# Optimization experiments

Measured on AMD Instinct MI355X. Metric: run time of the kernel, lower is better.

The kernel has to match this reference:

```python
import jax, jax.numpy as jnp
import numpy as np

D_MODEL = 512
EPS = 1e-5


def setup_inputs() -> dict:
    key = jax.random.key(0)
    k1, k2, k3 = jax.random.split(key, 3)
    B, N, D = 8, 2048, D_MODEL
    output = jax.random.normal(k1, (B, N, D), dtype=jnp.float32)
    # multiplicative 0/1 float mask over the [B, N, N] score matrix
    slf_attn_mask = jax.random.randint(k2, (B, N, N), 0, 2).astype(jnp.float32)
    # nn.Linear(d_model, d_model): weight [out, in], xavier-uniform; bias zeros-ish
    limit = float(np.sqrt(6.0 / (D + D)))
    W = jax.random.uniform(k3, (D, D), dtype=jnp.float32, minval=-limit, maxval=limit)
    b = jnp.zeros((D,), dtype=jnp.float32)
    return {"output": output, "slf_attn_mask": slf_attn_mask, "W": W, "b": b}


def reference(output, slf_attn_mask, W, b):
    temperature = jnp.asarray(D_MODEL, output.dtype) ** 0.5
    # scores: [B, N, N] = (q / temp) @ k^T, then multiplicative mask
    attn = jnp.einsum("bnd,bmd->bnm", output / temperature, output) * slf_attn_mask
    # F.normalize(p=2, dim=-1, eps=1e-5): x / max(||x||_2, eps)
    norm = jnp.sqrt(jnp.sum(attn * attn, axis=-1, keepdims=True))
    attn = attn / jnp.maximum(norm, EPS)
    # values: elu(Linear(output)), Linear uses W @ x + b with W [out, in]
    v = jax.nn.elu(jnp.einsum("bnd,ed->bne", output, W) + b)
    return jnp.einsum("bnm,bme->bne", attn, v)
```

## Files before the change

### kernel.cpp

```cpp
#include <hip/hip_runtime.h>
#include <hip/hip_bf16.h>

#define NSEQ 2048
#define DM 512
#define BATCH 8
#define GTOT (BATCH * NSEQ)
#define INV_T 0.044194173824159216f
#define EPSN 1e-5f

typedef __bf16 bf16_t;
typedef bf16_t bf16x8 __attribute__((ext_vector_type(8)));
typedef float f32x16 __attribute__((ext_vector_type(16)));
typedef unsigned short u16;
typedef unsigned int u32;
typedef unsigned long long u64;

__device__ __forceinline__ u16 f2bf(float f) {
    u32 u = __builtin_bit_cast(u32, f);
    u32 r = (u + 0x7FFFu + ((u >> 16) & 1u)) >> 16;
    return (u16)r;
}

__device__ __forceinline__ void async16(const u16* g, u16* l) {
    __builtin_amdgcn_global_load_lds(
        (const __attribute__((address_space(1))) u32*)g,
        (__attribute__((address_space(3))) u32*)l, 16, 0, 0);
}

__device__ __forceinline__ bf16x8 fragld(const u16* t, int row, int kc) {
    return *(const bf16x8*)(t + row * 32 + ((kc ^ ((row >> 1) & 3)) << 3));
}

#define MFMA32(a, b, c) __builtin_amdgcn_mfma_f32_32x32x16_bf16(a, b, c, 0, 0, 0)
#define ROWOFF(reg, lh) (((reg) & 3) + 8 * ((reg) >> 2) + 4 * (lh))

#define STAGE(Ag, ldA, Bg, ldB, k0)                                                    \
    do {                                                                               \
        async16((Ag) + (long)rA0 * (ldA) + (k0) + kcg * 8, Ab + u0 * 512 + lane * 8);  \
        async16((Ag) + (long)(rA0 + 16) * (ldA) + (k0) + kcg * 8, Ab + (u0 + 1) * 512 + lane * 8); \
        async16((Bg) + (long)rA0 * (ldB) + (k0) + kcg * 8, Bb + u0 * 512 + lane * 8);  \
        async16((Bg) + (long)(rA0 + 16) * (ldB) + (k0) + kcg * 8, Bb + (u0 + 1) * 512 + lane * 8); \
    } while (0)

__global__ __launch_bounds__(256) void k_convert(
    const float* __restrict__ X, const float* __restrict__ W,
    const float* __restrict__ mask,
    u16* __restrict__ Kbf, u16* __restrict__ Wbf,
    float* __restrict__ ssbuf, u64* __restrict__ Mbits) {
    const long NK = (long)GTOT * DM / 4;
    const long NW = (long)DM * DM / 4;
    const long NS = GTOT / 4;
    const long NM = (long)BATCH * NSEQ * NSEQ / 4;
    long i = (long)blockIdx.x * 256 + threadIdx.x;
    if (i < NK) {
        float4 f = ((const float4*)X)[i];
        ushort4 o;
        o.x = f2bf(f.x); o.y = f2bf(f.y); o.z = f2bf(f.z); o.w = f2bf(f.w);
        ((ushort4*)Kbf)[i] = o;
    } else if (i < NK + NW) {
        long j = i - NK;
        float4 f = ((const float4*)W)[j];
        ushort4 o;
        o.x = f2bf(f.x); o.y = f2bf(f.y); o.z = f2bf(f.z); o.w = f2bf(f.w);
        ((ushort4*)Wbf)[j] = o;
    } else if (i < NK + NW + NS) {
        ((float4*)ssbuf)[i - NK - NW] = (float4){0.f, 0.f, 0.f, 0.f};
    } else if (i < NK + NW + NS + NM) {
        long j4 = i - NK - NW - NS;
        int lane = threadIdx.x & 63;
        long wb = (j4 >> 6) << 6;
        long elembase = wb * 4;
#pragma unroll
        for (int it = 0; it < 4; ++it) {
            float f = mask[elembase + it * 64 + lane];
            u64 bb = __ballot(f != 0.f);
            if (lane == 0) Mbits[((wb >> 6) << 2) + it] = bb;
        }
    }
}

__global__ __launch_bounds__(256, 4) void k_sgemm(
    const u16* __restrict__ Kbf, const u32* __restrict__ Mw,
    u16* __restrict__ Sbuf, float* __restrict__ ssbuf) {
    __shared__ __attribute__((aligned(16))) u16 Ab[4096], Bb[4096];
    const int tid = threadIdx.x, wave = tid >> 6, lane = tid & 63;
    const int l31 = lane & 31, lh = lane >> 5;
    const int wy = wave >> 1, wx = wave & 1;
    const int b = blockIdx.z;
    const int M0 = blockIdx.y * 128, N0 = blockIdx.x * 128;
    const u16* Ag = Kbf + (long)(b * NSEQ + M0) * DM;
    const u16* Bg = Kbf + (long)(b * NSEQ + N0) * DM;
    const u32* Mb = Mw + (long)b * NSEQ * 64;

    const int u0 = wave * 2;
    const int rA0 = u0 * 16 + (lane >> 2);
    const int kcg = (lane & 3) ^ ((lane >> 3) & 3);

    f32x16 acc[2][2];
#pragma unroll
    for (int i = 0; i < 2; ++i)
#pragma unroll
        for (int j = 0; j < 2; ++j)
#pragma unroll
            for (int e = 0; e < 16; ++e) acc[i][j][e] = 0.f;

    for (int kt = 0; kt < 16; ++kt) {
        const int k0 = kt * 32;
        __syncthreads();
        STAGE(Ag, DM, Bg, DM, k0);
        __syncthreads();
#pragma unroll
        for (int ks = 0; ks < 2; ++ks) {
            const int kc = ks * 2 + lh;
            bf16x8 a0 = fragld(Ab, wy * 64 + l31, kc);
            bf16x8 a1 = fragld(Ab, wy * 64 + 32 + l31, kc);
            bf16x8 b0 = fragld(Bb, wx * 64 + l31, kc);
            bf16x8 b1 = fragld(Bb, wx * 64 + 32 + l31, kc);
            acc[0][0] = MFMA32(a0, b0, acc[0][0]);
            acc[0][1] = MFMA32(a0, b1, acc[0][1]);
            acc[1][0] = MFMA32(a1, b0, acc[1][0]);
            acc[1][1] = MFMA32(a1, b1, acc[1][1]);
        }
    }
#pragma unroll
    for (int mi = 0; mi < 2; ++mi) {
#pragma unroll
        for (int reg = 0; reg < 16; ++reg) {
            int rl = M0 + wy * 64 + mi * 32 + ROWOFF(reg, lh);
            long rg = (long)b * NSEQ + rl;
            float v = 0.f;
#pragma unroll
            for (int ni = 0; ni < 2; ++ni) {
                int cg = N0 + wx * 64 + ni * 32 + l31;
                u32 w = Mb[(long)rl * 64 + (cg >> 5)];
                float s = ((w >> l31) & 1u) ? acc[mi][ni][reg] * INV_T : 0.f;
                v += s * s;
                Sbuf[rg * NSEQ + cg] = f2bf(s);
            }
            v += __shfl_xor(v, 1, 32);
            v += __shfl_xor(v, 2, 32);
            v += __shfl_xor(v, 4, 32);
            v += __shfl_xor(v, 8, 32);
            v += __shfl_xor(v, 16, 32);
            if (l31 == 0) atomicAdd(&ssbuf[rg], v);
        }
    }
}

__global__ __launch_bounds__(256, 4) void k_vgemm(
    const u16* __restrict__ Wbf, const u16* __restrict__ Kbf,
    const float* __restrict__ bias, u16* __restrict__ vT) {
    __shared__ __attribute__((aligned(16))) u16 Ab[4096], Bb[4096];
    const int tid = threadIdx.x, wave = tid >> 6, lane = tid & 63;
    const int l31 = lane & 31, lh = lane >> 5;
    const int wy = wave >> 1, wx = wave & 1;
    const int M0 = blockIdx.y * 128, N0 = blockIdx.x * 128;
    const u16* Ag = Wbf + (long)M0 * DM;
    const u16* Bg = Kbf + (long)N0 * DM;

    const int u0 = wave * 2;
    const int rA0 = u0 * 16 + (lane >> 2);
    const int kcg = (lane & 3) ^ ((lane >> 3) & 3);

    f32x16 acc[2][2];
#pragma unroll
    for (int i = 0; i < 2; ++i)
#pragma unroll
        for (int j = 0; j < 2; ++j)
#pragma unroll
            for (int e = 0; e < 16; ++e) acc[i][j][e] = 0.f;

    for (int kt = 0; kt < 16; ++kt) {
        const int k0 = kt * 32;
        __syncthreads();
        STAGE(Ag, DM, Bg, DM, k0);
        __syncthreads();
#pragma unroll
        for (int ks = 0; ks < 2; ++ks) {
            const int kc = ks * 2 + lh;
            bf16x8 a0 = fragld(Ab, wy * 64 + l31, kc);
            bf16x8 a1 = fragld(Ab, wy * 64 + 32 + l31, kc);
            bf16x8 b0 = fragld(Bb, wx * 64 + l31, kc);
            bf16x8 b1 = fragld(Bb, wx * 64 + 32 + l31, kc);
            acc[0][0] = MFMA32(a0, b0, acc[0][0]);
            acc[0][1] = MFMA32(a0, b1, acc[0][1]);
            acc[1][0] = MFMA32(a1, b0, acc[1][0]);
            acc[1][1] = MFMA32(a1, b1, acc[1][1]);
        }
    }
#pragma unroll
    for (int mi = 0; mi < 2; ++mi) {
#pragma unroll
        for (int reg = 0; reg < 16; ++reg) {
            int e = M0 + wy * 64 + mi * 32 + ROWOFF(reg, lh);
            float bv = bias[e];
#pragma unroll
            for (int ni = 0; ni < 2; ++ni) {
                int g = N0 + wx * 64 + ni * 32 + l31;
                float x = acc[mi][ni][reg] + bv;
                float v = x > 0.f ? x : (__expf(x) - 1.f);
                vT[(long)e * GTOT + g] = f2bf(v);
            }
        }
    }
}

__global__ __launch_bounds__(256, 4) void k_pv(
    const u16* __restrict__ Sbuf, const u16* __restrict__ vT,
    const float* __restrict__ ssbuf, float* __restrict__ Out) {
    __shared__ __attribute__((aligned(16))) u16 Ab[4096], Bb[4096];
    __shared__ float sc[128];
    const int tid = threadIdx.x, wave = tid >> 6, lane = tid & 63;
    const int l31 = lane & 31, lh = lane >> 5;
    const int wy = wave >> 1, wx = wave & 1;
    const int b = blockIdx.z;
    const int M0 = blockIdx.y * 128, N0 = blockIdx.x * 128;
    const u16* Ag = Sbuf + (long)(b * NSEQ + M0) * NSEQ;
    const u16* Bg = vT + (long)N0 * GTOT + b * NSEQ;

    if (tid < 128) {
        float v = ssbuf[b * NSEQ + M0 + tid];
        sc[tid] = 1.f / fmaxf(sqrtf(v), EPSN);
    }

    const int u0 = wave * 2;
    const int rA0 = u0 * 16 + (lane >> 2);
    const int kcg = (lane & 3) ^ ((lane >> 3) & 3);

    f32x16 acc[2][2];
#pragma unroll
    for (int i = 0; i < 2; ++i)
#pragma unroll
        for (int j = 0; j < 2; ++j)
#pragma unroll
            for (int e = 0; e < 16; ++e) acc[i][j][e] = 0.f;

    for (int kt = 0; kt < 64; ++kt) {
        const int k0 = kt * 32;
        __syncthreads();
        STAGE(Ag, NSEQ, Bg, GTOT, k0);
        __syncthreads();
#pragma unroll
        for (int ks = 0; ks < 2; ++ks) {
            const int kc = ks * 2 + lh;
            bf16x8 a0 = fragld(Ab, wy * 64 + l31, kc);
            bf16x8 a1 = fragld(Ab, wy * 64 + 32 + l31, kc);
            bf16x8 b0 = fragld(Bb, wx * 64 + l31, kc);
            bf16x8 b1 = fragld(Bb, wx * 64 + 32 + l31, kc);
            acc[0][0] = MFMA32(a0, b0, acc[0][0]);
            acc[0][1] = MFMA32(a0, b1, acc[0][1]);
            acc[1][0] = MFMA32(a1, b0, acc[1][0]);
            acc[1][1] = MFMA32(a1, b1, acc[1][1]);
        }
    }
#pragma unroll
    for (int mi = 0; mi < 2; ++mi) {
#pragma unroll
        for (int reg = 0; reg < 16; ++reg) {
            int rl = wy * 64 + mi * 32 + ROWOFF(reg, lh);
            float s = sc[rl];
            float* op = Out + ((long)b * NSEQ + M0 + rl) * DM;
#pragma unroll
            for (int ni = 0; ni < 2; ++ni) {
                int d = N0 + wx * 64 + ni * 32 + l31;
                op[d] = acc[mi][ni][reg] * s;
            }
        }
    }
}

extern "C" void kernel_launch(void* const* d_in, const int* in_sizes, int n_in,
                              void* d_out, int out_size, void* d_ws, size_t ws_size,
                              hipStream_t stream) {
    const float* X = (const float*)d_in[0];
    const float* mask = (const float*)d_in[1];
    const float* W = (const float*)d_in[2];
    const float* bias = (const float*)d_in[3];
    float* out = (float*)d_out;

    char* ws = (char*)d_ws;
    u16* Kbf = (u16*)ws;
    u16* Wbf = (u16*)(ws + 16777216);
    u16* vT = (u16*)(ws + 17301504);
    u16* Sbuf = (u16*)(ws + 34078720);
    float* ssbuf = (float*)(ws + 101187584);
    u64* Mbits = (u64*)(ws + 101253120);

    k_convert<<<41232, 256, 0, stream>>>(X, W, mask, Kbf, Wbf, ssbuf, Mbits);
    k_vgemm<<<dim3(128, 4), 256, 0, stream>>>(Wbf, Kbf, bias, vT);
    k_sgemm<<<dim3(16, 16, 8), 256, 0, stream>>>(Kbf, (const u32*)Mbits, Sbuf, ssbuf);
    k_pv<<<dim3(4, 16, 8), 256, 0, stream>>>(Sbuf, vT, ssbuf, out);
}
```

Baseline: 370.9 us.

## Double GEMM K-tile to 64 and split mask packing into float4 kernel

All three bf16 MFMA GEMMs now stage 64-wide K tiles instead of 32, using a new 8-way XOR swizzle. This halves the number of barrier pairs per K loop and doubles the work done between syncs, at the cost of twice the LDS per block, which may limit occupancy. The mask bit-packing moves out of the convert kernel into its own kernel. That kernel reads float4 per thread and assembles the 64-bit words through shared-memory nibbles, replacing scalar per-lane loads with a ballot.

After: 348.1 us. 1.07x faster.

```diff
diff --git a/kernel.cpp b/kernel.cpp
--- a/kernel.cpp
+++ b/kernel.cpp
@@ -13,6 +13,7 @@
 typedef float f32x16 __attribute__((ext_vector_type(16)));
 typedef unsigned short u16;
 typedef unsigned int u32;
+typedef unsigned char u8;
 typedef unsigned long long u64;
 
 __device__ __forceinline__ u16 f2bf(float f) {
@@ -27,30 +28,29 @@
         (__attribute__((address_space(3))) u32*)l, 16, 0, 0);
 }
 
-__device__ __forceinline__ bf16x8 fragld(const u16* t, int row, int kc) {
-    return *(const bf16x8*)(t + row * 32 + ((kc ^ ((row >> 1) & 3)) << 3));
+__device__ __forceinline__ bf16x8 fragld64(const u16* t, int row, int kc) {
+    return *(const bf16x8*)(t + row * 64 + ((kc ^ ((row >> 1) & 7)) << 3));
 }
 
 #define MFMA32(a, b, c) __builtin_amdgcn_mfma_f32_32x32x16_bf16(a, b, c, 0, 0, 0)
 #define ROWOFF(reg, lh) (((reg) & 3) + 8 * ((reg) >> 2) + 4 * (lh))
 
-#define STAGE(Ag, ldA, Bg, ldB, k0)                                                    \
-    do {                                                                               \
-        async16((Ag) + (long)rA0 * (ldA) + (k0) + kcg * 8, Ab + u0 * 512 + lane * 8);  \
-        async16((Ag) + (long)(rA0 + 16) * (ldA) + (k0) + kcg * 8, Ab + (u0 + 1) * 512 + lane * 8); \
-        async16((Bg) + (long)rA0 * (ldB) + (k0) + kcg * 8, Bb + u0 * 512 + lane * 8);  \
-        async16((Bg) + (long)(rA0 + 16) * (ldB) + (k0) + kcg * 8, Bb + (u0 + 1) * 512 + lane * 8); \
+#define STAGE64(Ag, ldA, Bg, ldB, k0)                                            \
+    do {                                                                         \
+        _Pragma("unroll") for (int j = 0; j < 4; ++j) {                          \
+            const int cg = (lane & 7) ^ ((j * 4 + (lane >> 4)) & 7);             \
+            const int dst = (wave * 4 + j) * 512 + lane * 8;                     \
+            async16((Ag) + (long)(rS + j * 8) * (ldA) + (k0) + cg * 8, Ab + dst);\
+            async16((Bg) + (long)(rS + j * 8) * (ldB) + (k0) + cg * 8, Bb + dst);\
+        }                                                                        \
     } while (0)
 
 __global__ __launch_bounds__(256) void k_convert(
     const float* __restrict__ X, const float* __restrict__ W,
-    const float* __restrict__ mask,
-    u16* __restrict__ Kbf, u16* __restrict__ Wbf,
-    float* __restrict__ ssbuf, u64* __restrict__ Mbits) {
+    u16* __restrict__ Kbf, u16* __restrict__ Wbf, float* __restrict__ ssbuf) {
     const long NK = (long)GTOT * DM / 4;
     const long NW = (long)DM * DM / 4;
     const long NS = GTOT / 4;
-    const long NM = (long)BATCH * NSEQ * NSEQ / 4;
     long i = (long)blockIdx.x * 256 + threadIdx.x;
     if (i < NK) {
         float4 f = ((const float4*)X)[i];
@@ -65,24 +65,31 @@
         ((ushort4*)Wbf)[j] = o;
     } else if (i < NK + NW + NS) {
         ((float4*)ssbuf)[i - NK - NW] = (float4){0.f, 0.f, 0.f, 0.f};
-    } else if (i < NK + NW + NS + NM) {
-        long j4 = i - NK - NW - NS;
-        int lane = threadIdx.x & 63;
-        long wb = (j4 >> 6) << 6;
-        long elembase = wb * 4;
-#pragma unroll
-        for (int it = 0; it < 4; ++it) {
-            float f = mask[elembase + it * 64 + lane];
-            u64 bb = __ballot(f != 0.f);
-            if (lane == 0) Mbits[((wb >> 6) << 2) + it] = bb;
-        }
+    }
+}
+
+__global__ __launch_bounds__(256) void k_maskpack(
+    const float* __restrict__ mask, u64* __restrict__ Mbits) {
+    __shared__ u8 nib[256];
+    const int tid = threadIdx.x;
+    const long fbase = (long)blockIdx.x * 256 + tid;
+    float4 f = ((const float4*)mask)[fbase];
+    unsigned n = (f.x != 0.f ? 1u : 0u) | (f.y != 0.f ? 2u : 0u) |
+                 (f.z != 0.f ? 4u : 0u) | (f.w != 0.f ? 8u : 0u);
+    nib[tid] = (u8)n;
+    __syncthreads();
+    if (tid < 16) {
+        u64 w = 0;
+#pragma unroll
+        for (int i = 0; i < 16; ++i) w |= (u64)nib[tid * 16 + i] << (i * 4);
+        Mbits[(long)blockIdx.x * 16 + tid] = w;
     }
 }
 
 __global__ __launch_bounds__(256, 4) void k_sgemm(
     const u16* __restrict__ Kbf, const u32* __restrict__ Mw,
     u16* __restrict__ Sbuf, float* __restrict__ ssbuf) {
-    __shared__ __attribute__((aligned(16))) u16 Ab[4096], Bb[4096];
+    __shared__ __attribute__((aligned(16))) u16 Ab[8192], Bb[8192];
     const int tid = threadIdx.x, wave = tid >> 6, lane = tid & 63;
     const int l31 = lane & 31, lh = lane >> 5;
     const int wy = wave >> 1, wx = wave & 1;
@@ -92,9 +99,7 @@
     const u16* Bg = Kbf + (long)(b * NSEQ + N0) * DM;
     const u32* Mb = Mw + (long)b * NSEQ * 64;
 
-    const int u0 = wave * 2;
-    const int rA0 = u0 * 16 + (lane >> 2);
-    const int kcg = (lane & 3) ^ ((lane >> 3) & 3);
+    const int rS = wave * 32 + (lane >> 3);
 
     f32x16 acc[2][2];
 #pragma unroll
@@ -104,18 +109,18 @@
 #pragma unroll
             for (int e = 0; e < 16; ++e) acc[i][j][e] = 0.f;
 
-    for (int kt = 0; kt < 16; ++kt) {
-        const int k0 = kt * 32;
-        __syncthreads();
-        STAGE(Ag, DM, Bg, DM, k0);
-        __syncthreads();
-#pragma unroll
-        for (int ks = 0; ks < 2; ++ks) {
+    for (int kt = 0; kt < 8; ++kt) {
+        const int k0 = kt * 64;
+        __syncthreads();
+        STAGE64(Ag, DM, Bg, DM, k0);
+        __syncthreads();
+#pragma unroll
+        for (int ks = 0; ks < 4; ++ks) {
             const int kc = ks * 2 + lh;
-            bf16x8 a0 = fragld(Ab, wy * 64 + l31, kc);
-            bf16x8 a1 = fragld(Ab, wy * 64 + 32 + l31, kc);
-            bf16x8 b0 = fragld(Bb, wx * 64 + l31, kc);
-            bf16x8 b1 = fragld(Bb, wx * 64 + 32 + l31, kc);
+            bf16x8 a0 = fragld64(Ab, wy * 64 + l31, kc);
+            bf16x8 a1 = fragld64(Ab, wy * 64 + 32 + l31, kc);
+            bf16x8 b0 = fragld64(Bb, wx * 64 + l31, kc);
+            bf16x8 b1 = fragld64(Bb, wx * 64 + 32 + l31, kc);
             acc[0][0] = MFMA32(a0, b0, acc[0][0]);
             acc[0][1] = MFMA32(a0, b1, acc[0][1]);
             acc[1][0] = MFMA32(a1, b0, acc[1][0]);
@@ -150,7 +155,7 @@
 __global__ __launch_bounds__(256, 4) void k_vgemm(
     const u16* __restrict__ Wbf, const u16* __restrict__ Kbf,
     const float* __restrict__ bias, u16* __restrict__ vT) {
-    __shared__ __attribute__((aligned(16))) u16 Ab[4096], Bb[4096];
+    __shared__ __attribute__((aligned(16))) u16 Ab[8192], Bb[8192];
     const int tid = threadIdx.x, wave = tid >> 6, lane = tid & 63;
     const int l31 = lane & 31, lh = lane >> 5;
     const int wy = wave >> 1, wx = wave & 1;
@@ -158,9 +163,7 @@
     const u16* Ag = Wbf + (long)M0 * DM;
     const u16* Bg = Kbf + (long)N0 * DM;
 
-    const int u0 = wave * 2;
-    const int rA0 = u0 * 16 + (lane >> 2);
-    const int kcg = (lane & 3) ^ ((lane >> 3) & 3);
+    const int rS = wave * 32 + (lane >> 3);
 
     f32x16 acc[2][2];
 #pragma unroll
@@ -170,18 +173,18 @@
 #pragma unroll
             for (int e = 0; e < 16; ++e) acc[i][j][e] = 0.f;
 
-    for (int kt = 0; kt < 16; ++kt) {
-        const int k0 = kt * 32;
-        __syncthreads();
-        STAGE(Ag, DM, Bg, DM, k0);
-        __syncthreads();
-#pragma unroll
-        for (int ks = 0; ks < 2; ++ks) {
+    for (int kt = 0; kt < 8; ++kt) {
+        const int k0 = kt * 64;
+        __syncthreads();
+        STAGE64(Ag, DM, Bg, DM, k0);
+        __syncthreads();
+#pragma unroll
+        for (int ks = 0; ks < 4; ++ks) {
             const int kc = ks * 2 + lh;
-            bf16x8 a0 = fragld(Ab, wy * 64 + l31, kc);
-            bf16x8 a1 = fragld(Ab, wy * 64 + 32 + l31, kc);
-            bf16x8 b0 = fragld(Bb, wx * 64 + l31, kc);
-            bf16x8 b1 = fragld(Bb, wx * 64 + 32 + l31, kc);
+            bf16x8 a0 = fragld64(Ab, wy * 64 + l31, kc);
+            bf16x8 a1 = fragld64(Ab, wy * 64 + 32 + l31, kc);
+            bf16x8 b0 = fragld64(Bb, wx * 64 + l31, kc);
+            bf16x8 b1 = fragld64(Bb, wx * 64 + 32 + l31, kc);
             acc[0][0] = MFMA32(a0, b0, acc[0][0]);
             acc[0][1] = MFMA32(a0, b1, acc[0][1]);
             acc[1][0] = MFMA32(a1, b0, acc[1][0]);
@@ -208,7 +211,7 @@
 __global__ __launch_bounds__(256, 4) void k_pv(
     const u16* __restrict__ Sbuf, const u16* __restrict__ vT,
     const float* __restrict__ ssbuf, float* __restrict__ Out) {
-    __shared__ __attribute__((aligned(16))) u16 Ab[4096], Bb[4096];
+    __shared__ __attribute__((aligned(16))) u16 Ab[8192], Bb[8192];
     __shared__ float sc[128];
     const int tid = threadIdx.x, wave = tid >> 6, lane = tid & 63;
     const int l31 = lane & 31, lh = lane >> 5;
@@ -223,9 +226,7 @@
         sc[tid] = 1.f / fmaxf(sqrtf(v), EPSN);
     }
 
-    const int u0 = wave * 2;
-    const int rA0 = u0 * 16 + (lane >> 2);
-    const int kcg = (lane & 3) ^ ((lane >> 3) & 3);
+    const int rS = wave * 32 + (lane >> 3);
 
     f32x16 acc[2][2];
 #pragma unroll
@@ -235,18 +236,18 @@
 #pragma unroll
             for (int e = 0; e < 16; ++e) acc[i][j][e] = 0.f;
 
-    for (int kt = 0; kt < 64; ++kt) {
-        const int k0 = kt * 32;
-        __syncthreads();
-        STAGE(Ag, NSEQ, Bg, GTOT, k0);
-        __syncthreads();
-#pragma unroll
-        for (int ks = 0; ks < 2; ++ks) {
+    for (int kt = 0; kt < 32; ++kt) {
+        const int k0 = kt * 64;
+        __syncthreads();
+        STAGE64(Ag, NSEQ, Bg, GTOT, k0);
+        __syncthreads();
+#pragma unroll
+        for (int ks = 0; ks < 4; ++ks) {
             const int kc = ks * 2 + lh;
-            bf16x8 a0 = fragld(Ab, wy * 64 + l31, kc);
-            bf16x8 a1 = fragld(Ab, wy * 64 + 32 + l31, kc);
-            bf16x8 b0 = fragld(Bb, wx * 64 + l31, kc);
-            bf16x8 b1 = fragld(Bb, wx * 64 + 32 + l31, kc);
+            bf16x8 a0 = fragld64(Ab, wy * 64 + l31, kc);
+            bf16x8 a1 = fragld64(Ab, wy * 64 + 32 + l31, kc);
+            bf16x8 b0 = fragld64(Bb, wx * 64 + l31, kc);
+            bf16x8 b1 = fragld64(Bb, wx * 64 + 32 + l31, kc);
             acc[0][0] = MFMA32(a0, b0, acc[0][0]);
             acc[0][1] = MFMA32(a0, b1, acc[0][1]);
             acc[1][0] = MFMA32(a1, b0, acc[1][0]);
@@ -286,7 +287,8 @@
     float* ssbuf = (float*)(ws + 101187584);
     u64* Mbits = (u64*)(ws + 101253120);
 
-    k_convert<<<41232, 256, 0, stream>>>(X, W, mask, Kbf, Wbf, ssbuf, Mbits);
+    k_convert<<<8464, 256, 0, stream>>>(X, W, Kbf, Wbf, ssbuf);
+    k_maskpack<<<32768, 256, 0, stream>>>(mask, Mbits);
     k_vgemm<<<dim3(128, 4), 256, 0, stream>>>(Wbf, Kbf, bias, vT);
     k_sgemm<<<dim3(16, 16, 8), 256, 0, stream>>>(Kbf, (const u32*)Mbits, Sbuf, ssbuf);
     k_pv<<<dim3(4, 16, 8), 256, 0, stream>>>(Sbuf, vT, ssbuf, out);
```
